# Performance work log

Measured on AMD Instinct MI355X. Metric: run time of the kernel, lower is better.

The kernel has to match this reference:

```python
import jax, jax.numpy as jnp
import numpy as np

L, B = 512, 1
NODE_DIM, EDGE_DIM = 256, 128
MLP_DIM = NODE_DIM + EDGE_DIM  # 384 ('concat' outer op)
LN_EPS = 1e-5


def setup_inputs() -> dict:
    key = jax.random.key(0)
    ks = jax.random.split(key, 12)
    s = 0.02
    return {
        "x": jax.random.normal(ks[0], (L, B, NODE_DIM), dtype=jnp.float32),
        "z": jax.random.normal(ks[1], (B, L, L, EDGE_DIM), dtype=jnp.float32),
        "Wd": jax.random.normal(ks[2], (NODE_DIM // 2, NODE_DIM), dtype=jnp.float32) * s,
        "bd": jnp.zeros((NODE_DIM // 2,), dtype=jnp.float32),
        "W1": jax.random.normal(ks[3], (MLP_DIM, MLP_DIM), dtype=jnp.float32) * s,
        "b1": jnp.zeros((MLP_DIM,), dtype=jnp.float32),
        "W2": jax.random.normal(ks[4], (MLP_DIM, MLP_DIM), dtype=jnp.float32) * s,
        "b2": jnp.zeros((MLP_DIM,), dtype=jnp.float32),
        "Wo": jax.random.normal(ks[5], (EDGE_DIM, MLP_DIM), dtype=jnp.float32) * s,
        "bo": jnp.zeros((EDGE_DIM,), dtype=jnp.float32),
        "gamma": jnp.ones((EDGE_DIM,), dtype=jnp.float32),
        "beta": jnp.zeros((EDGE_DIM,), dtype=jnp.float32),
    }


def reference(x, z, Wd, bd, W1, b1, W2, b2, Wo, bo, gamma, beta):
    # down-project nodes: x [L,B,nd] -> x_down [B,L,nd//2]
    x_down = jnp.swapaxes(x @ Wd.T + bd, 0, 1)
    n = x_down.shape[1]
    # outer 'concat': edge_bias [B,L,L,nd]
    row = jnp.broadcast_to(x_down[:, :, None, :], (x_down.shape[0], n, n, x_down.shape[-1]))
    col = jnp.broadcast_to(x_down[:, None, :, :], (x_down.shape[0], n, n, x_down.shape[-1]))
    edge_bias = jnp.concatenate([row, col], axis=-1)
    z_in = jnp.concatenate([edge_bias, z], axis=-1)  # [B,L,L,MLP_DIM]
    # edge MLP (Linear-ReLU-Linear-ReLU) + residual, then out linear
    h = jax.nn.relu(z_in @ W1.T + b1)
    h = jax.nn.relu(h @ W2.T + b2)
    out = (h + z_in) @ Wo.T + bo  # [B,L,L,EDGE_DIM]
    # LayerNorm over last dim
    mu = out.mean(axis=-1, keepdims=True)
    var = out.var(axis=-1, keepdims=True)
    return (out - mu) * jax.lax.rsqrt(var + LN_EPS) * gamma + beta
```

## Files before the change

kernel.cpp:

```cpp
#include <hip/hip_runtime.h>


using bf16x8 = __attribute__((ext_vector_type(8))) __bf16;
using f32x16 = __attribute__((ext_vector_type(16))) float;

#define LPAD 392
#define OPAD 132

__device__ inline unsigned short f2bf(float f) {
    union { float f; unsigned int u; } v; v.f = f;
    unsigned int r = v.u + 0x7fffu + ((v.u >> 16) & 1u);
    return (unsigned short)(r >> 16);
}
__device__ inline float bf2f(unsigned short h) {
    union { unsigned int u; float f; } v; v.u = ((unsigned int)h) << 16;
    return v.f;
}

__global__ void k_prep(const float* __restrict__ x, const float* __restrict__ Wd,
                       const float* __restrict__ bd, unsigned short* __restrict__ xd,
                       const float* __restrict__ W1, const float* __restrict__ W2,
                       const float* __restrict__ Wo,
                       unsigned short* __restrict__ W1s, unsigned short* __restrict__ W2s,
                       unsigned short* __restrict__ Wos) {
    if (blockIdx.x < 256) {
        __shared__ float sx[2][256];
        const int half = threadIdx.x >> 7;
        const int t = threadIdx.x & 127;
        const int i = blockIdx.x * 2 + half;
        if (t < 64) *(float4*)&sx[half][t * 4] = *(const float4*)&x[i * 256 + t * 4];
        __syncthreads();
        const float* wr = &Wd[t * 256];
        const float* xr = sx[half];
        float sum = 0.f;
#pragma unroll 8
        for (int k = 0; k < 256; k += 4) {
            float4 wv = *(const float4*)&wr[k];
            float4 xv = *(const float4*)&xr[k];
            sum += wv.x * xv.x + wv.y * xv.y + wv.z * xv.z + wv.w * xv.w;
        }
        xd[i * 128 + t] = f2bf(sum + bd[t]);
    } else {
        const int b = blockIdx.x - 256;
        const float* W; unsigned short* dst; int c;
        if (b < 72)       { W = W1; dst = W1s; c = b * 256 + threadIdx.x; }
        else if (b < 144) { W = W2; dst = W2s; c = (b - 72) * 256 + threadIdx.x; }
        else              { W = Wo; dst = Wos; c = (b - 144) * 256 + threadIdx.x; }
        int lane = c & 63;
        int ks = (c >> 6) % 24;
        int nt = c / (24 * 64);
        int n = nt * 32 + (lane & 31);
        int k0 = ks * 16 + ((lane >> 5) << 3);
        const float* src = &W[n * 384 + k0];
        unsigned short tmp[8];
#pragma unroll
        for (int j = 0; j < 8; ++j) tmp[j] = f2bf(src[j]);
        *(uint4*)&dst[(size_t)c * 8] = *(const uint4*)tmp;
    }
}

__global__ __launch_bounds__(768) void edge_main(
    const float* __restrict__ z, const unsigned short* __restrict__ xd,
    const unsigned short* __restrict__ W1s, const unsigned short* __restrict__ W2s,
    const unsigned short* __restrict__ Wos,
    const float* __restrict__ b1, const float* __restrict__ b2,
    const float* __restrict__ bo, const float* __restrict__ gamma,
    const float* __restrict__ beta, float* __restrict__ out)
{
    extern __shared__ char smem[];
    unsigned short* sA = (unsigned short*)smem;
    unsigned short* sH = (unsigned short*)(smem + 64 * LPAD * 2);
    float* sO = (float*)sH;

    const int tid = threadIdx.x;
    const int lane = tid & 63;
    const int w = tid >> 6;
    const int i = blockIdx.x >> 3;
    const int j0 = (blockIdx.x & 7) << 6;

    const int arow = lane & 31;
    const int kof = (lane >> 5) << 3;
    const int half2 = (lane >> 5) << 2;

    const int mt  = w & 1;
    const int ng  = w >> 1;
    const int rbase = mt << 5;

    for (int c = tid; c < 64 * 16; c += 768) {
        int r = c >> 4, cc = (c & 15) << 3;
        *(uint4*)&sA[r * LPAD + cc] = *(const uint4*)&xd[i * 128 + cc];
        *(uint4*)&sA[r * LPAD + 128 + cc] = *(const uint4*)&xd[(j0 + r) * 128 + cc];
    }
    for (int c = tid; c < 64 * 32; c += 768) {
        int r = c >> 5, cc = (c & 31) << 2;
        float4 v = *(const float4*)&z[((size_t)((i << 9) + j0 + r) << 7) + cc];
        ushort4 o;
        o.x = f2bf(v.x); o.y = f2bf(v.y); o.z = f2bf(v.z); o.w = f2bf(v.w);
        *(ushort4*)&sA[r * LPAD + 256 + cc] = o;
    }
    __syncthreads();

    {
        f32x16 acc0 = {}, acc1 = {};
#pragma unroll 6
        for (int ks = 0; ks < 24; ++ks) {
            int k = ks * 16 + kof;
            bf16x8 a  = *(const bf16x8*)&sA[(rbase + arow) * LPAD + k];
            bf16x8 b0 = *(const bf16x8*)&W1s[(size_t)(((ng    ) * 24 + ks) * 64 + lane) * 8];
            bf16x8 bb1 = *(const bf16x8*)&W1s[(size_t)(((ng + 6) * 24 + ks) * 64 + lane) * 8];
            acc0 = __builtin_amdgcn_mfma_f32_32x32x16_bf16(a, b0, acc0, 0, 0, 0);
            acc1 = __builtin_amdgcn_mfma_f32_32x32x16_bf16(a, bb1, acc1, 0, 0, 0);
        }
        const int colA = ng * 32 + arow;
        const int colB = (ng + 6) * 32 + arow;
        const float biasA = b1[colA];
        const float biasB = b1[colB];
#pragma unroll
        for (int rg = 0; rg < 16; ++rg) {
            int rr = rbase + half2 + (rg & 3) + ((rg >> 2) << 3);
            float v0 = acc0[rg] + biasA; v0 = v0 > 0.f ? v0 : 0.f;
            float v1 = acc1[rg] + biasB; v1 = v1 > 0.f ? v1 : 0.f;
            sH[rr * LPAD + colA] = f2bf(v0);
            sH[rr * LPAD + colB] = f2bf(v1);
        }
    }
    __syncthreads();

    {
        f32x16 acc0 = {}, acc1 = {};
#pragma unroll 6
        for (int ks = 0; ks < 24; ++ks) {
            int k = ks * 16 + kof;
            bf16x8 a  = *(const bf16x8*)&sH[(rbase + arow) * LPAD + k];
            bf16x8 b0 = *(const bf16x8*)&W2s[(size_t)(((ng    ) * 24 + ks) * 64 + lane) * 8];
            bf16x8 bb1 = *(const bf16x8*)&W2s[(size_t)(((ng + 6) * 24 + ks) * 64 + lane) * 8];
            acc0 = __builtin_amdgcn_mfma_f32_32x32x16_bf16(a, b0, acc0, 0, 0, 0);
            acc1 = __builtin_amdgcn_mfma_f32_32x32x16_bf16(a, bb1, acc1, 0, 0, 0);
        }
        const int colA = ng * 32 + arow;
        const int colB = (ng + 6) * 32 + arow;
        const float biasA = b2[colA];
        const float biasB = b2[colB];
#pragma unroll
        for (int rg = 0; rg < 16; ++rg) {
            int rr = rbase + half2 + (rg & 3) + ((rg >> 2) << 3);
            float v0 = acc0[rg] + biasA; v0 = v0 > 0.f ? v0 : 0.f;
            float v1 = acc1[rg] + biasB; v1 = v1 > 0.f ? v1 : 0.f;
            float r0 = bf2f(sA[rr * LPAD + colA]);
            float r1 = bf2f(sA[rr * LPAD + colB]);
            sA[rr * LPAD + colA] = f2bf(v0 + r0);
            sA[rr * LPAD + colB] = f2bf(v1 + r1);
        }
    }
    __syncthreads();

    if (w < 8) {
        const int mt3 = w >> 2;
        const int nt3 = w & 3;
        f32x16 acc = {};
#pragma unroll 6
        for (int ks = 0; ks < 24; ++ks) {
            int k = ks * 16 + kof;
            bf16x8 a0 = *(const bf16x8*)&sA[(arow + mt3 * 32) * LPAD + k];
            bf16x8 b = *(const bf16x8*)&Wos[(size_t)((nt3 * 24 + ks) * 64 + lane) * 8];
            acc = __builtin_amdgcn_mfma_f32_32x32x16_bf16(a0, b, acc, 0, 0, 0);
        }
        int col = nt3 * 32 + arow;
        float bias = bo[col];
#pragma unroll
        for (int rg = 0; rg < 16; ++rg) {
            int rr = mt3 * 32 + half2 + (rg & 3) + ((rg >> 2) << 3);
            sO[rr * OPAD + col] = acc[rg] + bias;
        }
    }
    __syncthreads();

    if (tid < 256) {
        const int r = tid >> 2;
        const int q = tid & 3;
        float s = 0.f, ss = 0.f;
#pragma unroll
        for (int ii = 0; ii < 32; ++ii) {
            float v = sO[r * OPAD + q + (ii << 2)];
            s += v; ss += v * v;
        }
        s += __shfl_xor(s, 1);  ss += __shfl_xor(ss, 1);
        s += __shfl_xor(s, 2);  ss += __shfl_xor(ss, 2);
        const float mean = s * (1.f / 128.f);
        const float var = ss * (1.f / 128.f) - mean * mean;
        const float rstd = rsqrtf(var + 1e-5f);
        float* po = &out[((size_t)((i << 9) + j0 + r)) << 7];
#pragma unroll
        for (int ii = 0; ii < 8; ++ii) {
            int c0 = q * 32 + (ii << 2);
            float4 v = *(const float4*)&sO[r * OPAD + c0];
            float4 g = *(const float4*)&gamma[c0];
            float4 bb = *(const float4*)&beta[c0];
            float4 o;
            o.x = (v.x - mean) * rstd * g.x + bb.x;
            o.y = (v.y - mean) * rstd * g.y + bb.y;
            o.z = (v.z - mean) * rstd * g.z + bb.z;
            o.w = (v.w - mean) * rstd * g.w + bb.w;
            *(float4*)&po[c0] = o;
        }
    }
}

extern "C" void kernel_launch(void* const* d_in, const int* in_sizes, int n_in,
                              void* d_out, int out_size, void* d_ws, size_t ws_size,
                              hipStream_t stream) {
    const float* x     = (const float*)d_in[0];
    const float* z     = (const float*)d_in[1];
    const float* Wd    = (const float*)d_in[2];
    const float* bd    = (const float*)d_in[3];
    const float* W1    = (const float*)d_in[4];
    const float* b1    = (const float*)d_in[5];
    const float* W2    = (const float*)d_in[6];
    const float* b2    = (const float*)d_in[7];
    const float* Wo    = (const float*)d_in[8];
    const float* bo    = (const float*)d_in[9];
    const float* gamma = (const float*)d_in[10];
    const float* beta  = (const float*)d_in[11];
    float* out = (float*)d_out;

    unsigned short* xd  = (unsigned short*)d_ws;
    unsigned short* W1s = (unsigned short*)((char*)d_ws + 131072);
    unsigned short* W2s = (unsigned short*)((char*)d_ws + 425984);
    unsigned short* Wos = (unsigned short*)((char*)d_ws + 720896);

    hipLaunchKernelGGL(k_prep, dim3(424), dim3(256), 0, stream,
                       x, Wd, bd, xd, W1, W2, Wo, W1s, W2s, Wos);

    const size_t smem = (size_t)(64 * LPAD * 2) * 2;
    hipLaunchKernelGGL(edge_main, dim3(4096), dim3(768), smem, stream,
                       z, xd, W1s, W2s, Wos, b1, b2, bo, gamma, beta, out);
}
```

Baseline: 529.4 us.

## Restructure LDS layout with XOR swizzle and drop broadcast row copy

Replaces the padded row-major LDS tiles with XOR-swizzled, unpadded x/z/H buffers. The broadcast x_down[i] segment is no longer stored per row and is read straight from global memory. The H buffer is reused for the residual-plus-hidden tile and then aliased by the output tile, which cuts LDS from about 100KB to 80KB. The aim is fewer bank conflicts and a smaller LDS footprint, possibly allowing more residency. The cost is extra barriers and more scattered global reads in the first GEMM.

```diff
diff --git a/kernel.cpp b/kernel.cpp
--- a/kernel.cpp
+++ b/kernel.cpp
@@ -4,7 +4,6 @@
 using bf16x8 = __attribute__((ext_vector_type(8))) __bf16;
 using f32x16 = __attribute__((ext_vector_type(16))) float;
 
-#define LPAD 392
 #define OPAD 132
 
 __device__ inline unsigned short f2bf(float f) {
@@ -68,9 +67,10 @@
     const float* __restrict__ beta, float* __restrict__ out)
 {
     extern __shared__ char smem[];
-    unsigned short* sA = (unsigned short*)smem;
-    unsigned short* sH = (unsigned short*)(smem + 64 * LPAD * 2);
-    float* sO = (float*)sH;
+    char* sXb = smem;
+    char* sZb = smem + 16384;
+    char* sHb = smem + 32768;
+    float* sO = (float*)(smem + 32768);
 
     const int tid = threadIdx.x;
     const int lane = tid & 63;
@@ -85,92 +85,114 @@
     const int mt  = w & 1;
     const int ng  = w >> 1;
     const int rbase = mt << 5;
+    const int row = rbase + arow;
+    const int rswz = (row & 7) << 4;
 
     for (int c = tid; c < 64 * 16; c += 768) {
-        int r = c >> 4, cc = (c & 15) << 3;
-        *(uint4*)&sA[r * LPAD + cc] = *(const uint4*)&xd[i * 128 + cc];
-        *(uint4*)&sA[r * LPAD + 128 + cc] = *(const uint4*)&xd[(j0 + r) * 128 + cc];
+        int r = c >> 4, cb = (c & 15) << 4;
+        *(uint4*)(sXb + ((r * 256 + cb) ^ ((r & 7) << 4))) =
+            *(const uint4*)&xd[(j0 + r) * 128 + (cb >> 1)];
     }
     for (int c = tid; c < 64 * 32; c += 768) {
         int r = c >> 5, cc = (c & 31) << 2;
         float4 v = *(const float4*)&z[((size_t)((i << 9) + j0 + r) << 7) + cc];
         ushort4 o;
         o.x = f2bf(v.x); o.y = f2bf(v.y); o.z = f2bf(v.z); o.w = f2bf(v.w);
-        *(ushort4*)&sA[r * LPAD + 256 + cc] = o;
-    }
-    __syncthreads();
+        *(ushort4*)(sZb + ((r * 256 + (cc << 1)) ^ ((r & 7) << 4))) = o;
+    }
+    __syncthreads();
+
+    const int colA = ng * 32 + arow;
+    const int colB = colA + 192;
 
     {
         f32x16 acc0 = {}, acc1 = {};
-#pragma unroll 6
+#pragma unroll
         for (int ks = 0; ks < 24; ++ks) {
-            int k = ks * 16 + kof;
-            bf16x8 a  = *(const bf16x8*)&sA[(rbase + arow) * LPAD + k];
-            bf16x8 b0 = *(const bf16x8*)&W1s[(size_t)(((ng    ) * 24 + ks) * 64 + lane) * 8];
+            const int k = ks * 16 + kof;
+            bf16x8 a;
+            if (ks < 8)
+                a = *(const bf16x8*)&xd[i * 128 + k];
+            else if (ks < 16)
+                a = *(const bf16x8*)(sXb + ((row * 256 + (k - 128) * 2) ^ rswz));
+            else
+                a = *(const bf16x8*)(sZb + ((row * 256 + (k - 256) * 2) ^ rswz));
+            bf16x8 b0  = *(const bf16x8*)&W1s[(size_t)(((ng    ) * 24 + ks) * 64 + lane) * 8];
             bf16x8 bb1 = *(const bf16x8*)&W1s[(size_t)(((ng + 6) * 24 + ks) * 64 + lane) * 8];
-            acc0 = __builtin_amdgcn_mfma_f32_32x32x16_bf16(a, b0, acc0, 0, 0, 0);
+            acc0 = __builtin_amdgcn_mfma_f32_32x32x16_bf16(a, b0,  acc0, 0, 0, 0);
             acc1 = __builtin_amdgcn_mfma_f32_32x32x16_bf16(a, bb1, acc1, 0, 0, 0);
         }
-        const int colA = ng * 32 + arow;
-        const int colB = (ng + 6) * 32 + arow;
         const float biasA = b1[colA];
         const float biasB = b1[colB];
 #pragma unroll
         for (int rg = 0; rg < 16; ++rg) {
             int rr = rbase + half2 + (rg & 3) + ((rg >> 2) << 3);
+            int rsw = (rr & 7) << 4;
             float v0 = acc0[rg] + biasA; v0 = v0 > 0.f ? v0 : 0.f;
             float v1 = acc1[rg] + biasB; v1 = v1 > 0.f ? v1 : 0.f;
-            sH[rr * LPAD + colA] = f2bf(v0);
-            sH[rr * LPAD + colB] = f2bf(v1);
+            *(unsigned short*)(sHb + ((rr * 768 + colA * 2) ^ rsw)) = f2bf(v0);
+            *(unsigned short*)(sHb + ((rr * 768 + colB * 2) ^ rsw)) = f2bf(v1);
         }
     }
     __syncthreads();
 
     {
         f32x16 acc0 = {}, acc1 = {};
-#pragma unroll 6
+#pragma unroll
         for (int ks = 0; ks < 24; ++ks) {
-            int k = ks * 16 + kof;
-            bf16x8 a  = *(const bf16x8*)&sH[(rbase + arow) * LPAD + k];
-            bf16x8 b0 = *(const bf16x8*)&W2s[(size_t)(((ng    ) * 24 + ks) * 64 + lane) * 8];
+            const int k = ks * 16 + kof;
+            bf16x8 a  = *(const bf16x8*)(sHb + ((row * 768 + k * 2) ^ rswz));
+            bf16x8 b0  = *(const bf16x8*)&W2s[(size_t)(((ng    ) * 24 + ks) * 64 + lane) * 8];
             bf16x8 bb1 = *(const bf16x8*)&W2s[(size_t)(((ng + 6) * 24 + ks) * 64 + lane) * 8];
-            acc0 = __builtin_amdgcn_mfma_f32_32x32x16_bf16(a, b0, acc0, 0, 0, 0);
+            acc0 = __builtin_amdgcn_mfma_f32_32x32x16_bf16(a, b0,  acc0, 0, 0, 0);
             acc1 = __builtin_amdgcn_mfma_f32_32x32x16_bf16(a, bb1, acc1, 0, 0, 0);
         }
-        const int colA = ng * 32 + arow;
-        const int colB = (ng + 6) * 32 + arow;
+        __syncthreads();
+
         const float biasA = b2[colA];
         const float biasB = b2[colB];
+        const bool aGlob = (ng <= 3);
+        float resAg = 0.f;
+        if (aGlob) resAg = bf2f(xd[i * 128 + colA]);
 #pragma unroll
         for (int rg = 0; rg < 16; ++rg) {
             int rr = rbase + half2 + (rg & 3) + ((rg >> 2) << 3);
+            int rsw = (rr & 7) << 4;
             float v0 = acc0[rg] + biasA; v0 = v0 > 0.f ? v0 : 0.f;
             float v1 = acc1[rg] + biasB; v1 = v1 > 0.f ? v1 : 0.f;
-            float r0 = bf2f(sA[rr * LPAD + colA]);
-            float r1 = bf2f(sA[rr * LPAD + colB]);
-            sA[rr * LPAD + colA] = f2bf(v0 + r0);
-            sA[rr * LPAD + colB] = f2bf(v1 + r1);
-        }
-    }
-    __syncthreads();
-
+            float r0 = aGlob ? resAg
+                 : bf2f(*(const unsigned short*)(sXb + ((rr * 256 + (colA - 128) * 2) ^ rsw)));
+            float r1 = (ng <= 1)
+                 ? bf2f(*(const unsigned short*)(sXb + ((rr * 256 + (colB - 128) * 2) ^ rsw)))
+                 : bf2f(*(const unsigned short*)(sZb + ((rr * 256 + (colB - 256) * 2) ^ rsw)));
+            *(unsigned short*)(sHb + ((rr * 768 + colA * 2) ^ rsw)) = f2bf(v0 + r0);
+            *(unsigned short*)(sHb + ((rr * 768 + colB * 2) ^ rsw)) = f2bf(v1 + r1);
+        }
+    }
+    __syncthreads();
+
+    f32x16 acc3 = {};
+    const int mt3 = w >> 2;
+    const int nt3 = w & 3;
     if (w < 8) {
-        const int mt3 = w >> 2;
-        const int nt3 = w & 3;
-        f32x16 acc = {};
-#pragma unroll 6
+        const int row3 = mt3 * 32 + arow;
+        const int r3sw = (row3 & 7) << 4;
+#pragma unroll
         for (int ks = 0; ks < 24; ++ks) {
-            int k = ks * 16 + kof;
-            bf16x8 a0 = *(const bf16x8*)&sA[(arow + mt3 * 32) * LPAD + k];
+            const int k = ks * 16 + kof;
+            bf16x8 a = *(const bf16x8*)(sHb + ((row3 * 768 + k * 2) ^ r3sw));
             bf16x8 b = *(const bf16x8*)&Wos[(size_t)((nt3 * 24 + ks) * 64 + lane) * 8];
-            acc = __builtin_amdgcn_mfma_f32_32x32x16_bf16(a0, b, acc, 0, 0, 0);
-        }
+            acc3 = __builtin_amdgcn_mfma_f32_32x32x16_bf16(a, b, acc3, 0, 0, 0);
+        }
+    }
+    __syncthreads();
+    if (w < 8) {
         int col = nt3 * 32 + arow;
         float bias = bo[col];
 #pragma unroll
         for (int rg = 0; rg < 16; ++rg) {
             int rr = mt3 * 32 + half2 + (rg & 3) + ((rg >> 2) << 3);
-            sO[rr * OPAD + col] = acc[rg] + bias;
+            sO[rr * OPAD + col] = acc3[rg] + bias;
         }
     }
     __syncthreads();
@@ -231,7 +253,7 @@
     hipLaunchKernelGGL(k_prep, dim3(424), dim3(256), 0, stream,
                        x, Wd, bd, xd, W1, W2, Wo, W1s, W2s, Wos);
 
-    const size_t smem = (size_t)(64 * LPAD * 2) * 2;
+    const size_t smem = 81920;
     hipLaunchKernelGGL(edge_main, dim3(4096), dim3(768), smem, stream,
                        z, xd, W1s, W2s, Wos, b1, b2, bo, gamma, beta, out);
 }
```

After: 533.9 us. Within noise of the previous version (+0.8%).
